# Optimization experiments

Measured on AMD Instinct MI355X. Metric: run time of the kernel, lower is better.

## Reference

```python
import jax, jax.numpy as jnp
import numpy as np

B, NPG, DEG = 128, 400, 16
N, E = B * NPG, B * NPG * DEG
E_PER = E // B
K1, K2, K3 = 360, 324, 292  # ceil(0.9*400), ceil(0.9*360), ceil(0.9*324)
EPS = 1e-5


def setup_inputs() -> dict:
    key = jax.random.key(0)
    ks = jax.random.split(key, 48)
    # edges constrained within each graph (contiguous equal-size graphs)
    g = jnp.repeat(jnp.arange(B, dtype=jnp.int32), E_PER)
    src = jax.random.randint(ks[0], (E,), 0, NPG, dtype=jnp.int32) + g * NPG
    dst = jax.random.randint(ks[1], (E,), 0, NPG, dtype=jnp.int32) + g * NPG
    inp = {
        'x': jax.random.normal(ks[2], (N, 64), dtype=jnp.float32),
        'edge_index': jnp.stack([src, dst]),
        'batch': jnp.repeat(jnp.arange(B, dtype=jnp.int32), NPG),
    }
    def glorot(k, a, b):
        lim = float(np.sqrt(6.0 / (a + b)))
        return jax.random.uniform(k, (a, b), minval=-lim, maxval=lim, dtype=jnp.float32)
    conv_dims = [(64, 32), (32, 64), (64, 128), (128, 128)]
    for i, (a, b) in enumerate(conv_dims, 1):
        inp[f'W{i}'] = glorot(ks[2 + i], a, b)
        inp[f'b{i}'] = jnp.zeros((b,), jnp.float32)
    for i, d in zip((1, 2, 3), (32, 64, 128)):
        inp[f'p{i}'] = jax.random.uniform(ks[8 + i], (d,), minval=-1.0, maxval=1.0, dtype=jnp.float32) / float(np.sqrt(d))
    lin_dims = [(128, 64), (64, 64), (64, 32), (32, 16), (16, 1)]
    for i, (a, b) in enumerate(lin_dims, 1):
        inp[f'Lw{i}'] = glorot(ks[12 + i], a, b)
        inp[f'Lb{i}'] = jnp.zeros((b,), jnp.float32)
    for i, d in enumerate((64, 64, 32, 16), 1):
        inp[f'g{i}'] = jnp.ones((d,), jnp.float32)
        inp[f'be{i}'] = jnp.zeros((d,), jnp.float32)
    return inp


def _gcn(x, src, dst, emask, nmask, W, b):
    h = x @ W
    deg = nmask + jax.ops.segment_sum(emask, dst, num_segments=N)
    dinv = jnp.where(deg > 0, jax.lax.rsqrt(deg), 0.0)
    norm = dinv[src] * dinv[dst] * emask
    agg = jax.ops.segment_sum(h[src] * norm[:, None], dst, num_segments=N)
    agg = agg + h * (dinv * dinv * nmask)[:, None]  # self-loop term
    return (agg + b) * nmask[:, None]


def _topk_pool(x, nmask, p, k):
    # PyG TopKPooling: score = x.p/||p||, keep top-k per graph, x *= tanh(score)
    score = (x @ p) / jnp.linalg.norm(p)
    sel = jnp.where(nmask > 0, score, -jnp.inf).reshape(B, NPG)
    _, idx = jax.lax.top_k(sel, k)
    gidx = (idx + (jnp.arange(B) * NPG)[:, None]).reshape(-1)
    new_mask = jnp.zeros((N,), x.dtype).at[gidx].set(1.0)
    return x * (jnp.tanh(score) * new_mask)[:, None], new_mask


def reference(x, edge_index, batch, W1, b1, p1, W2, b2, p2, W3, b3, p3, W4, b4,
              Lw1, Lb1, Lw2, Lb2, Lw3, Lb3, Lw4, Lb4, Lw5, Lb5,
              g1, be1, g2, be2, g3, be3, g4, be4):
    src, dst = edge_index[0], edge_index[1]
    nmask = jnp.ones((N,), jnp.float32)
    emask = jnp.ones((E,), jnp.float32)
    x = jax.nn.relu(_gcn(x, src, dst, emask, nmask, W1, b1))
    x, nmask = _topk_pool(x, nmask, p1, K1)
    emask = emask * nmask[src] * nmask[dst]
    x = jax.nn.relu(_gcn(x, src, dst, emask, nmask, W2, b2))
    x, nmask = _topk_pool(x, nmask, p2, K2)
    emask = emask * nmask[src] * nmask[dst]
    x = jax.nn.relu(_gcn(x, src, dst, emask, nmask, W3, b3))
    x, nmask = _topk_pool(x, nmask, p3, K3)
    emask = emask * nmask[src] * nmask[dst]
    x = jax.nn.relu(_gcn(x, src, dst, emask, nmask, W4, b4))
    h = x.reshape(B, NPG, -1).max(axis=1)
    def lin_bn(h, W, bb, ga, be):
        h = h @ W + bb
        m = h.mean(0)
        v = h.var(0)  # biased, matches BatchNorm1d training normalization
        return jax.nn.relu(ga * (h - m) / jnp.sqrt(v + EPS) + be)
    h = lin_bn(h, Lw1, Lb1, g1, be1)
    h = lin_bn(h, Lw2, Lb2, g2, be2)
    h = lin_bn(h, Lw3, Lb3, g3, be3)
    h = lin_bn(h, Lw4, Lb4, g4, be4)
    return h @ Lw5 + Lb5
```

## Files before the change

### kernel.cpp

```cpp
#include <hip/hip_runtime.h>
#include <math.h>

#define NNODES 51200
#define BGRAPHS 128
#define NPG 400
#define NEDGES 819200
#define EPG 6400
#define SLP 7680

__global__ __launch_bounds__(512) void csr_build_kernel(
    const int* __restrict__ src, const int* __restrict__ dst,
    unsigned short* __restrict__ slg, int* __restrict__ gsg, int* __restrict__ gcg,
    float* __restrict__ nmask, float* __restrict__ dinv, float* __restrict__ sc,
    float* __restrict__ hp) {
    __shared__ int deg[NPG];
    __shared__ int incl[512];
    __shared__ int gs[NPG];
    __shared__ int cur[NPG];
    const int g = blockIdx.x, t = threadIdx.x;
    for (int i = t; i < NPG; i += 512) deg[i] = 0;
    if (t < 128) hp[g * 128 + t] = 0.0f;
    __syncthreads();
    for (int e = t; e < EPG; e += 512)
        atomicAdd(&deg[dst[g * EPG + e] - g * NPG], 1);
    __syncthreads();
    const int d = (t < NPG) ? deg[t] : 0;
    const int p = (d + 3) >> 2;
    incl[t] = p;
    __syncthreads();
    for (int off = 1; off < 512; off <<= 1) {
        int add = (t >= off) ? incl[t - off] : 0;
        __syncthreads();
        incl[t] += add;
        __syncthreads();
    }
    if (t < NPG) {
        const int gstart = incl[t] - p;
        gs[t] = gstart;
        gsg[g * NPG + t] = gstart;
        gcg[g * NPG + t] = p;
        cur[t] = gstart * 4;
        nmask[g * NPG + t] = 1.0f;
        const float dv = rsqrtf(1.0f + (float)d);
        dinv[g * NPG + t] = dv;
        sc[g * NPG + t] = dv;
    }
    __syncthreads();
    for (int e = t; e < EPG; e += 512) {
        int dl = dst[g * EPG + e] - g * NPG;
        int pos = atomicAdd(&cur[dl], 1);
        slg[g * SLP + pos] = (unsigned short)(src[g * EPG + e] - g * NPG);
    }
    __syncthreads();
    if (t < NPG) {
        const int end = (gs[t] + p) * 4;
        for (int i = cur[t]; i < end; i++) slg[g * SLP + i] = (unsigned short)NPG;
    }
}

template<int IN, int OUT, int MODE>
__global__ __launch_bounds__(256) void gemm_kernel(
    const float* __restrict__ X, const float* __restrict__ W,
    const float* __restrict__ bias, const float* __restrict__ nmask,
    float* __restrict__ H, const float* __restrict__ p,
    float* __restrict__ score, float* __restrict__ hp) {
    __shared__ __align__(16) float sX[64 * IN];
    __shared__ unsigned smax[256];
    const int row0 = blockIdx.x * 64;
    const int t = threadIdx.x;
    for (int i = t; i < 64 * IN / 4; i += 256)
        reinterpret_cast<float4*>(sX)[i] =
            reinterpret_cast<const float4*>(X + (size_t)row0 * IN)[i];
    if (MODE == 3) smax[t] = 0u;
    __syncthreads();
    constexpr int CG  = OUT / 4;
    constexpr int RG  = 256 / CG;
    constexpr int RPT = 64 / RG;
    const int c0 = (t % CG) * 4;
    const int r0 = (t / CG) * RPT;
    float acc[RPT][4];
#pragma unroll
    for (int r = 0; r < RPT; r++)
#pragma unroll
        for (int j = 0; j < 4; j++) acc[r][j] = 0.0f;
    for (int k4 = 0; k4 < IN / 4; k4++) {
        const float4 w0 = *reinterpret_cast<const float4*>(&W[(k4 * 4 + 0) * OUT + c0]);
        const float4 w1 = *reinterpret_cast<const float4*>(&W[(k4 * 4 + 1) * OUT + c0]);
        const float4 w2 = *reinterpret_cast<const float4*>(&W[(k4 * 4 + 2) * OUT + c0]);
        const float4 w3 = *reinterpret_cast<const float4*>(&W[(k4 * 4 + 3) * OUT + c0]);
#pragma unroll
        for (int r = 0; r < RPT; r++) {
            const float4 xv = *reinterpret_cast<const float4*>(&sX[(r0 + r) * IN + k4 * 4]);
            acc[r][0] += xv.x * w0.x + xv.y * w1.x + xv.z * w2.x + xv.w * w3.x;
            acc[r][1] += xv.x * w0.y + xv.y * w1.y + xv.z * w2.y + xv.w * w3.y;
            acc[r][2] += xv.x * w0.z + xv.y * w1.z + xv.z * w2.z + xv.w * w3.z;
            acc[r][3] += xv.x * w0.w + xv.y * w1.w + xv.z * w2.w + xv.w * w3.w;
        }
    }
    const int graph0 = row0 / 400;
    const int bnd = (graph0 + 1) * 400;
    float ps[RPT];
    float cmax[4] = {0.f, 0.f, 0.f, 0.f};
#pragma unroll
    for (int r = 0; r < RPT; r++) {
        const int row = row0 + r0 + r;
        float4 v = make_float4(acc[r][0], acc[r][1], acc[r][2], acc[r][3]);
        if (MODE >= 2) {
            const float4 b4 = *reinterpret_cast<const float4*>(&bias[c0]);
            const float m = nmask[row];
            v.x = fmaxf(v.x + b4.x, 0.0f) * m;
            v.y = fmaxf(v.y + b4.y, 0.0f) * m;
            v.z = fmaxf(v.z + b4.z, 0.0f) * m;
            v.w = fmaxf(v.w + b4.w, 0.0f) * m;
        }
        if (MODE != 3) *reinterpret_cast<float4*>(&H[(size_t)row * OUT + c0]) = v;
        if (MODE == 2) {
            const float4 p4 = *reinterpret_cast<const float4*>(&p[c0]);
            ps[r] = v.x * p4.x + v.y * p4.y + v.z * p4.z + v.w * p4.w;
        }
        if (MODE == 3) {
            cmax[0] = fmaxf(cmax[0], v.x);
            cmax[1] = fmaxf(cmax[1], v.y);
            cmax[2] = fmaxf(cmax[2], v.z);
            cmax[3] = fmaxf(cmax[3], v.w);
        }
    }
    if (MODE == 2) {
#pragma unroll
        for (int r = 0; r < RPT; r++) {
#pragma unroll
            for (int off = 1; off < CG; off <<= 1) ps[r] += __shfl_xor(ps[r], off);
        }
        if ((t % CG) == 0) {
#pragma unroll
            for (int r = 0; r < RPT; r++) score[row0 + r0 + r] = ps[r];
        }
    }
    if (MODE == 3) {
        const int seg = ((row0 + r0) >= bnd) ? 1 : 0;
        atomicMax(&smax[seg * 128 + c0 + 0], __float_as_uint(cmax[0]));
        atomicMax(&smax[seg * 128 + c0 + 1], __float_as_uint(cmax[1]));
        atomicMax(&smax[seg * 128 + c0 + 2], __float_as_uint(cmax[2]));
        atomicMax(&smax[seg * 128 + c0 + 3], __float_as_uint(cmax[3]));
        __syncthreads();
        unsigned* hpu = reinterpret_cast<unsigned*>(hp);
        if (t < 128) atomicMax(&hpu[graph0 * 128 + t], smax[t]);
        const int graph1 = (row0 + 63) / 400;
        if (graph1 != graph0 && t < 128) atomicMax(&hpu[graph1 * 128 + t], smax[128 + t]);
    }
}

template<int OUT, int NCH, int NS, bool EPI, bool SCORE>
__global__ __launch_bounds__(512) void gcn_agg_kernel(
    const float* __restrict__ H, float* __restrict__ Y,
    const float* __restrict__ dinv, const float* __restrict__ sc,
    const float* __restrict__ bias, const float* __restrict__ p,
    float* __restrict__ score,
    const unsigned short* __restrict__ slg, const int* __restrict__ gsg,
    const int* __restrict__ gcg) {
    __shared__ __align__(16) float Hl[(NPG + 1) * 36];
    __shared__ float dinvl[NPG];
    __shared__ int gsl[NPG];
    __shared__ int gcl[NPG];
    __shared__ unsigned long long sl64[SLP / 4];
    const unsigned short* sl = reinterpret_cast<const unsigned short*>(sl64);
    const int b   = blockIdx.x;
    const int g   = b / (NCH * NS);
    const int rem = b % (NCH * NS);
    const int f0  = (rem / NS) * 32;
    const int n0  = (rem % NS) * (NPG / NS);
    const int t   = threadIdx.x;

    for (int i = t; i < NPG; i += 512) {
        dinvl[i] = dinv[g * NPG + i];
        gsl[i] = gsg[g * NPG + i];
        gcl[i] = gcg[g * NPG + i];
    }
    for (int i = t; i < SLP / 4; i += 512)
        sl64[i] = reinterpret_cast<const unsigned long long*>(slg + (size_t)g * SLP)[i];
    if (t < 36) Hl[NPG * 36 + t] = 0.0f;
    for (int i = t; i < NPG * 8; i += 512) {
        const int n = i >> 3, q = i & 7;
        const float s = sc[g * NPG + n];
        float4 v = *reinterpret_cast<const float4*>(&H[(size_t)(g * NPG + n) * OUT + f0 + q * 4]);
        v.x *= s; v.y *= s; v.z *= s; v.w *= s;
        *reinterpret_cast<float4*>(&Hl[n * 36 + q * 4]) = v;
    }
    __syncthreads();

    const int wave = t >> 6, lane = t & 63;
    const int sub = lane >> 3, f4 = lane & 7;
    constexpr int NPB = NPG / NS;
    for (int n = n0 + wave * 8 + sub; n < n0 + NPB; n += 64) {
        const float di = dinvl[n];
        if (di == 0.0f) continue;
        const int g0 = gsl[n], g1 = g0 + gcl[n];
        float4 acc = *reinterpret_cast<const float4*>(&Hl[n * 36 + f4 * 4]);
        for (int gg = g0; gg < g1; ++gg) {
            const unsigned long long q = *reinterpret_cast<const unsigned long long*>(&sl[gg * 4]);
            const int s0 = (int)(q & 0xFFFF), s1 = (int)((q >> 16) & 0xFFFF);
            const int s2 = (int)((q >> 32) & 0xFFFF), s3 = (int)(q >> 48);
            const float4 a = *reinterpret_cast<const float4*>(&Hl[s0 * 36 + f4 * 4]);
            const float4 bb = *reinterpret_cast<const float4*>(&Hl[s1 * 36 + f4 * 4]);
            const float4 c = *reinterpret_cast<const float4*>(&Hl[s2 * 36 + f4 * 4]);
            const float4 dd = *reinterpret_cast<const float4*>(&Hl[s3 * 36 + f4 * 4]);
            acc.x += (a.x + bb.x) + (c.x + dd.x);
            acc.y += (a.y + bb.y) + (c.y + dd.y);
            acc.z += (a.z + bb.z) + (c.z + dd.z);
            acc.w += (a.w + bb.w) + (c.w + dd.w);
        }
        acc.x *= di; acc.y *= di; acc.z *= di; acc.w *= di;
        if (EPI) {
            const float4 b4 = *reinterpret_cast<const float4*>(&bias[f0 + f4 * 4]);
            acc.x = fmaxf(acc.x + b4.x, 0.0f);
            acc.y = fmaxf(acc.y + b4.y, 0.0f);
            acc.z = fmaxf(acc.z + b4.z, 0.0f);
            acc.w = fmaxf(acc.w + b4.w, 0.0f);
        }
        *reinterpret_cast<float4*>(&Y[(size_t)(g * NPG + n) * OUT + f0 + f4 * 4]) = acc;
        if (SCORE) {
            const float4 p4 = *reinterpret_cast<const float4*>(&p[f4 * 4]);
            float part = acc.x * p4.x + acc.y * p4.y + acc.z * p4.z + acc.w * p4.w;
            part += __shfl_xor(part, 1);
            part += __shfl_xor(part, 2);
            part += __shfl_xor(part, 4);
            if (f4 == 0) score[g * NPG + n] = part;
        }
    }
}

template<int DIM>
__global__ __launch_bounds__(512) void topk_kernel(
    const float* __restrict__ score, float* __restrict__ nmask,
    float* __restrict__ dinv, float* __restrict__ sc,
    const float* __restrict__ p, int K,
    const unsigned short* __restrict__ slg, const int* __restrict__ gsg,
    const int* __restrict__ gcg) {
    __shared__ float sval[512];
    __shared__ int   sidx[512];
    __shared__ float sraw[NPG];
    __shared__ float nml[NPG + 1];
    __shared__ unsigned long long sl64[SLP / 4];
    __shared__ int gsl[NPG];
    __shared__ int gcl[NPG];
    __shared__ float spnorm;
    const unsigned short* sl = reinterpret_cast<const unsigned short*>(sl64);
    const int g = blockIdx.x;
    const int t = threadIdx.x;
    for (int i = t; i < SLP / 4; i += 512)
        sl64[i] = reinterpret_cast<const unsigned long long*>(slg + (size_t)g * SLP)[i];
    for (int i = t; i < NPG; i += 512) {
        gsl[i] = gsg[g * NPG + i];
        gcl[i] = gcg[g * NPG + i];
    }
    if (t == 0) {
        float s = 0.0f;
        for (int j = 0; j < DIM; j++) s += p[j] * p[j];
        spnorm = sqrtf(s);
    }
    float v = -INFINITY;
    int ix = t;
    if (t < NPG) {
        const float raw = score[g * NPG + t];
        sraw[t] = raw;
        v = (nmask[g * NPG + t] > 0.0f) ? raw : -INFINITY;
    }
    __syncthreads();
    for (int kk = 2; kk <= 512; kk <<= 1) {
        for (int j = kk >> 1; j > 0; j >>= 1) {
            float vb; int ib;
            if (j >= 64) {
                sval[t] = v; sidx[t] = ix;
                __syncthreads();
                vb = sval[t ^ j]; ib = sidx[t ^ j];
                __syncthreads();
            } else {
                vb = __shfl_xor(v, j, 64);
                ib = __shfl_xor(ix, j, 64);
            }
            const bool ownFirst = (v > vb) || (v == vb && ix < ib);
            const bool lower = (t & j) == 0;
            const bool desc = (t & kk) == 0;
            const bool keepOwn = lower ? (desc == ownFirst) : (desc != ownFirst);
            if (!keepOwn) { v = vb; ix = ib; }
        }
    }
    if (t <= NPG) nml[t] = 0.0f;
    __syncthreads();
    if (t < K) nml[ix] = 1.0f;
    __syncthreads();
    if (t < NPG) nmask[g * NPG + t] = nml[t];
    for (int n = t; n < NPG; n += 512) {
        float dv = 0.0f;
        if (nml[n] > 0.0f) {
            float d = 1.0f;
            const int g0 = gsl[n], g1 = g0 + gcl[n];
            for (int gg = g0; gg < g1; ++gg) {
                const unsigned long long q = *reinterpret_cast<const unsigned long long*>(&sl[gg * 4]);
                d += nml[(int)(q & 0xFFFF)] + nml[(int)((q >> 16) & 0xFFFF)] +
                     nml[(int)((q >> 32) & 0xFFFF)] + nml[(int)(q >> 48)];
            }
            dv = rsqrtf(d);
        }
        dinv[g * NPG + n] = dv;
        sc[g * NPG + n] = (nml[n] > 0.0f) ? tanhf(sraw[n] / spnorm) * dv : 0.0f;
    }
}

template<int IN, int OUT>
__global__ __launch_bounds__(128) void head_layer_kernel(
    const float* __restrict__ A, const float* __restrict__ W,
    const float* __restrict__ b, const float* __restrict__ ga,
    const float* __restrict__ be, float* __restrict__ Y) {
    __shared__ float Al[128 * (IN + 1)];
    __shared__ float red[4];
    const int c = blockIdx.x, t = threadIdx.x;
    for (int i = t; i < 128 * IN; i += 128)
        Al[(i / IN) * (IN + 1) + (i % IN)] = A[i];
    __syncthreads();
    float acc = b[c];
#pragma unroll
    for (int j = 0; j < IN; j++) acc += Al[t * (IN + 1) + j] * W[j * OUT + c];
    float s1 = acc, s2 = acc * acc;
    for (int o = 32; o > 0; o >>= 1) {
        s1 += __shfl_down(s1, o, 64);
        s2 += __shfl_down(s2, o, 64);
    }
    if ((t & 63) == 0) { red[t >> 6] = s1; red[2 + (t >> 6)] = s2; }
    __syncthreads();
    const float S1 = red[0] + red[1], S2 = red[2] + red[3];
    const float m = S1 * (1.0f / 128.0f);
    const float var = S2 * (1.0f / 128.0f) - m * m;
    float val = ga[c] * (acc - m) * rsqrtf(var + 1e-5f) + be[c];
    Y[t * OUT + c] = fmaxf(val, 0.0f);
}

__global__ __launch_bounds__(128) void head_final_kernel(
    const float* __restrict__ A, const float* __restrict__ w,
    const float* __restrict__ b, float* __restrict__ out) {
    const int t = threadIdx.x;
    float acc = b[0];
#pragma unroll
    for (int j = 0; j < 16; j++) acc += A[t * 16 + j] * w[j];
    out[t] = acc;
}

extern "C" void kernel_launch(void* const* d_in, const int* in_sizes, int n_in,
                              void* d_out, int out_size, void* d_ws, size_t ws_size,
                              hipStream_t stream) {
    (void)in_sizes; (void)n_in; (void)out_size; (void)ws_size;
    const float* x   = (const float*)d_in[0];
    const int*   ei  = (const int*)d_in[1];
    const float* W1  = (const float*)d_in[3];  const float* b1  = (const float*)d_in[4];
    const float* W2  = (const float*)d_in[5];  const float* b2  = (const float*)d_in[6];
    const float* W3  = (const float*)d_in[7];  const float* b3  = (const float*)d_in[8];
    const float* W4  = (const float*)d_in[9];  const float* b4  = (const float*)d_in[10];
    const float* p1  = (const float*)d_in[11];
    const float* p2  = (const float*)d_in[12];
    const float* p3  = (const float*)d_in[13];
    const float* Lw1 = (const float*)d_in[14]; const float* Lb1 = (const float*)d_in[15];
    const float* Lw2 = (const float*)d_in[16]; const float* Lb2 = (const float*)d_in[17];
    const float* Lw3 = (const float*)d_in[18]; const float* Lb3 = (const float*)d_in[19];
    const float* Lw4 = (const float*)d_in[20]; const float* Lb4 = (const float*)d_in[21];
    const float* Lw5 = (const float*)d_in[22]; const float* Lb5 = (const float*)d_in[23];
    const float* g1  = (const float*)d_in[24]; const float* be1 = (const float*)d_in[25];
    const float* g2  = (const float*)d_in[26]; const float* be2 = (const float*)d_in[27];
    const float* g3  = (const float*)d_in[28]; const float* be3 = (const float*)d_in[29];
    const float* g4  = (const float*)d_in[30]; const float* be4 = (const float*)d_in[31];

    const int* src = ei;
    const int* dst = ei + NEDGES;

    float* ws    = (float*)d_ws;
    float* hb    = ws;
    float* x0    = hb + (size_t)NNODES * 128;
    float* x1    = x0 + (size_t)NNODES * 128;
    float* nmask = x1 + (size_t)NNODES * 128;
    float* dinv  = nmask + NNODES;
    float* sc    = dinv + NNODES;
    float* scoreb= sc + NNODES;
    float* hp    = scoreb + NNODES;
    float* a1    = hp + 128 * 128;
    float* a2    = a1 + 128 * 64;
    float* a3    = a2 + 128 * 64;
    float* a4    = a3 + 128 * 32;
    unsigned short* slg = (unsigned short*)(a4 + 128 * 16);
    int* gsg = (int*)(slg + (size_t)BGRAPHS * SLP);
    int* gcg = gsg + (size_t)BGRAPHS * NPG;

    csr_build_kernel<<<BGRAPHS, 512, 0, stream>>>(src, dst, slg, gsg, gcg, nmask, dinv, sc, hp);

    gemm_kernel<64, 32, 0><<<NNODES / 64, 256, 0, stream>>>(x, W1, nullptr, nullptr, hb, nullptr, nullptr, nullptr);
    gcn_agg_kernel<32, 1, 2, true, true><<<BGRAPHS * 2, 512, 0, stream>>>(hb, x0, dinv, sc, b1, p1, scoreb, slg, gsg, gcg);
    topk_kernel<32><<<BGRAPHS, 512, 0, stream>>>(scoreb, nmask, dinv, sc, p1, 360, slg, gsg, gcg);

    gcn_agg_kernel<32, 1, 2, false, false><<<BGRAPHS * 2, 512, 0, stream>>>(x0, hb, dinv, sc, nullptr, nullptr, nullptr, slg, gsg, gcg);
    gemm_kernel<32, 64, 2><<<NNODES / 64, 256, 0, stream>>>(hb, W2, b2, nmask, x1, p2, scoreb, nullptr);
    topk_kernel<64><<<BGRAPHS, 512, 0, stream>>>(scoreb, nmask, dinv, sc, p2, 324, slg, gsg, gcg);

    gcn_agg_kernel<64, 2, 2, false, false><<<BGRAPHS * 4, 512, 0, stream>>>(x1, hb, dinv, sc, nullptr, nullptr, nullptr, slg, gsg, gcg);
    gemm_kernel<64, 128, 2><<<NNODES / 64, 256, 0, stream>>>(hb, W3, b3, nmask, x0, p3, scoreb, nullptr);
    topk_kernel<128><<<BGRAPHS, 512, 0, stream>>>(scoreb, nmask, dinv, sc, p3, 292, slg, gsg, gcg);

    gcn_agg_kernel<128, 4, 1, false, false><<<BGRAPHS * 4, 512, 0, stream>>>(x0, hb, dinv, sc, nullptr, nullptr, nullptr, slg, gsg, gcg);
    gemm_kernel<128, 128, 3><<<NNODES / 64, 256, 0, stream>>>(hb, W4, b4, nmask, x1, nullptr, nullptr, hp);

    head_layer_kernel<128, 64><<<64, 128, 0, stream>>>(hp, Lw1, Lb1, g1, be1, a1);
    head_layer_kernel<64, 64><<<64, 128, 0, stream>>>(a1, Lw2, Lb2, g2, be2, a2);
    head_layer_kernel<64, 32><<<32, 128, 0, stream>>>(a2, Lw3, Lb3, g3, be3, a3);
    head_layer_kernel<32, 16><<<16, 128, 0, stream>>>(a3, Lw4, Lb4, g4, be4, a4);
    head_final_kernel<<<1, 128, 0, stream>>>(a4, Lw5, Lb5, (float*)d_out);
}
```

Measured before the change: 204.9 us.

## Fuse top-k pooling into the following GCN aggregation kernel

Removes the standalone topk_kernel launches. Each aggregation block now recomputes the per-graph bitonic top-k, new node mask, degree normalisation and tanh score scale in shared memory before aggregating. The mask is double-buffered (nmA/nmB) so blocks can read the old mask while one block writes the new one. This removes three launches and the global round-trip for dinv and sc. In exchange, the sort is done redundantly by 2–4 blocks per graph, and each block's prologue gets longer.

```diff
diff --git a/kernel.cpp b/kernel.cpp
--- a/kernel.cpp
+++ b/kernel.cpp
@@ -150,19 +150,24 @@
     }
 }
 
-template<int OUT, int NCH, int NS, bool EPI, bool SCORE>
+template<int OUT, int NCH, int NS, bool EPI, bool SCORE, bool TOPK>
 __global__ __launch_bounds__(512) void gcn_agg_kernel(
     const float* __restrict__ H, float* __restrict__ Y,
-    const float* __restrict__ dinv, const float* __restrict__ sc,
-    const float* __restrict__ bias, const float* __restrict__ p,
-    float* __restrict__ score,
+    const float* __restrict__ dinv_g, const float* __restrict__ sc_g,
+    const float* __restrict__ bias,
+    const float* __restrict__ p_sc, float* __restrict__ score_out,
+    const float* __restrict__ scoreb_in, const float* __restrict__ nmask_in,
+    float* __restrict__ nmask_out, const float* __restrict__ p_pool,
+    int K, int PDIM,
     const unsigned short* __restrict__ slg, const int* __restrict__ gsg,
     const int* __restrict__ gcg) {
     __shared__ __align__(16) float Hl[(NPG + 1) * 36];
     __shared__ float dinvl[NPG];
+    __shared__ float scl[NPG];
     __shared__ int gsl[NPG];
     __shared__ int gcl[NPG];
     __shared__ unsigned long long sl64[SLP / 4];
+    __shared__ float misc[4];
     const unsigned short* sl = reinterpret_cast<const unsigned short*>(sl64);
     const int b   = blockIdx.x;
     const int g   = b / (NCH * NS);
@@ -172,20 +177,89 @@
     const int t   = threadIdx.x;
 
     for (int i = t; i < NPG; i += 512) {
-        dinvl[i] = dinv[g * NPG + i];
         gsl[i] = gsg[g * NPG + i];
         gcl[i] = gcg[g * NPG + i];
     }
     for (int i = t; i < SLP / 4; i += 512)
         sl64[i] = reinterpret_cast<const unsigned long long*>(slg + (size_t)g * SLP)[i];
-    if (t < 36) Hl[NPG * 36 + t] = 0.0f;
+
+    if (TOPK) {
+        float* sval = Hl;
+        int*   sidx = (int*)(Hl + 512);
+        float* sraw = Hl + 1024;
+        float* nml  = Hl + 1440;
+        if (t < 64) {
+            float s = 0.0f;
+            for (int j = t; j < PDIM; j += 64) s += p_pool[j] * p_pool[j];
+#pragma unroll
+            for (int o = 32; o > 0; o >>= 1) s += __shfl_xor(s, o, 64);
+            if (t == 0) misc[0] = sqrtf(s);
+        }
+        float v = -INFINITY;
+        int ix = t;
+        if (t < NPG) {
+            const float raw = scoreb_in[g * NPG + t];
+            sraw[t] = raw;
+            v = (nmask_in[g * NPG + t] > 0.0f) ? raw : -INFINITY;
+        }
+        __syncthreads();
+        for (int kk = 2; kk <= 512; kk <<= 1) {
+            for (int j = kk >> 1; j > 0; j >>= 1) {
+                float vb; int ib;
+                if (j >= 64) {
+                    sval[t] = v; sidx[t] = ix;
+                    __syncthreads();
+                    vb = sval[t ^ j]; ib = sidx[t ^ j];
+                    __syncthreads();
+                } else {
+                    vb = __shfl_xor(v, j, 64);
+                    ib = __shfl_xor(ix, j, 64);
+                }
+                const bool ownFirst = (v > vb) || (v == vb && ix < ib);
+                const bool lower = (t & j) == 0;
+                const bool desc = (t & kk) == 0;
+                const bool keepOwn = lower ? (desc == ownFirst) : (desc != ownFirst);
+                if (!keepOwn) { v = vb; ix = ib; }
+            }
+        }
+        if (t <= NPG) nml[t] = 0.0f;
+        __syncthreads();
+        if (t < K) nml[ix] = 1.0f;
+        __syncthreads();
+        if (rem == 0 && t < NPG) nmask_out[g * NPG + t] = nml[t];
+        const float spn = misc[0];
+        for (int n = t; n < NPG; n += 512) {
+            float dv = 0.0f;
+            if (nml[n] > 0.0f) {
+                float d = 1.0f;
+                const int g0 = gsl[n], g1 = g0 + gcl[n];
+                for (int gg = g0; gg < g1; ++gg) {
+                    const unsigned long long q = *reinterpret_cast<const unsigned long long*>(&sl[gg * 4]);
+                    d += nml[(int)(q & 0xFFFF)] + nml[(int)((q >> 16) & 0xFFFF)] +
+                         nml[(int)((q >> 32) & 0xFFFF)] + nml[(int)(q >> 48)];
+                }
+                dv = rsqrtf(d);
+            }
+            dinvl[n] = dv;
+            scl[n] = (nml[n] > 0.0f) ? tanhf(sraw[n] / spn) * dv : 0.0f;
+        }
+        __syncthreads();
+    } else {
+        for (int i = t; i < NPG; i += 512) {
+            dinvl[i] = dinv_g[g * NPG + i];
+            scl[i]   = sc_g[g * NPG + i];
+        }
+        __syncthreads();
+    }
+
     for (int i = t; i < NPG * 8; i += 512) {
         const int n = i >> 3, q = i & 7;
-        const float s = sc[g * NPG + n];
+        const float s = scl[n];
         float4 v = *reinterpret_cast<const float4*>(&H[(size_t)(g * NPG + n) * OUT + f0 + q * 4]);
         v.x *= s; v.y *= s; v.z *= s; v.w *= s;
         *reinterpret_cast<float4*>(&Hl[n * 36 + q * 4]) = v;
     }
+    if (t < 36) Hl[NPG * 36 + t] = 0.0f;
     __syncthreads();
 
     const int wave = t >> 6, lane = t & 63;
@@ -219,91 +293,13 @@
         }
         *reinterpret_cast<float4*>(&Y[(size_t)(g * NPG + n) * OUT + f0 + f4 * 4]) = acc;
         if (SCORE) {
-            const float4 p4 = *reinterpret_cast<const float4*>(&p[f4 * 4]);
+            const float4 p4 = *reinterpret_cast<const float4*>(&p_sc[f4 * 4]);
             float part = acc.x * p4.x + acc.y * p4.y + acc.z * p4.z + acc.w * p4.w;
             part += __shfl_xor(part, 1);
             part += __shfl_xor(part, 2);
             part += __shfl_xor(part, 4);
-            if (f4 == 0) score[g * NPG + n] = part;
-        }
-    }
-}
-
-template<int DIM>
-__global__ __launch_bounds__(512) void topk_kernel(
-    const float* __restrict__ score, float* __restrict__ nmask,
-    float* __restrict__ dinv, float* __restrict__ sc,
-    const float* __restrict__ p, int K,
-    const unsigned short* __restrict__ slg, const int* __restrict__ gsg,
-    const int* __restrict__ gcg) {
-    __shared__ float sval[512];
-    __shared__ int   sidx[512];
-    __shared__ float sraw[NPG];
-    __shared__ float nml[NPG + 1];
-    __shared__ unsigned long long sl64[SLP / 4];
-    __shared__ int gsl[NPG];
-    __shared__ int gcl[NPG];
-    __shared__ float spnorm;
-    const unsigned short* sl = reinterpret_cast<const unsigned short*>(sl64);
-    const int g = blockIdx.x;
-    const int t = threadIdx.x;
-    for (int i = t; i < SLP / 4; i += 512)
-        sl64[i] = reinterpret_cast<const unsigned long long*>(slg + (size_t)g * SLP)[i];
-    for (int i = t; i < NPG; i += 512) {
-        gsl[i] = gsg[g * NPG + i];
-        gcl[i] = gcg[g * NPG + i];
-    }
-    if (t == 0) {
-        float s = 0.0f;
-        for (int j = 0; j < DIM; j++) s += p[j] * p[j];
-        spnorm = sqrtf(s);
-    }
-    float v = -INFINITY;
-    int ix = t;
-    if (t < NPG) {
-        const float raw = score[g * NPG + t];
-        sraw[t] = raw;
-        v = (nmask[g * NPG + t] > 0.0f) ? raw : -INFINITY;
-    }
-    __syncthreads();
-    for (int kk = 2; kk <= 512; kk <<= 1) {
-        for (int j = kk >> 1; j > 0; j >>= 1) {
-            float vb; int ib;
-            if (j >= 64) {
-                sval[t] = v; sidx[t] = ix;
-                __syncthreads();
-                vb = sval[t ^ j]; ib = sidx[t ^ j];
-                __syncthreads();
-            } else {
-                vb = __shfl_xor(v, j, 64);
-                ib = __shfl_xor(ix, j, 64);
-            }
-            const bool ownFirst = (v > vb) || (v == vb && ix < ib);
-            const bool lower = (t & j) == 0;
-            const bool desc = (t & kk) == 0;
-            const bool keepOwn = lower ? (desc == ownFirst) : (desc != ownFirst);
-            if (!keepOwn) { v = vb; ix = ib; }
-        }
-    }
-    if (t <= NPG) nml[t] = 0.0f;
-    __syncthreads();
-    if (t < K) nml[ix] = 1.0f;
-    __syncthreads();
-    if (t < NPG) nmask[g * NPG + t] = nml[t];
-    for (int n = t; n < NPG; n += 512) {
-        float dv = 0.0f;
-        if (nml[n] > 0.0f) {
-            float d = 1.0f;
-            const int g0 = gsl[n], g1 = g0 + gcl[n];
-            for (int gg = g0; gg < g1; ++gg) {
-                const unsigned long long q = *reinterpret_cast<const unsigned long long*>(&sl[gg * 4]);
-                d += nml[(int)(q & 0xFFFF)] + nml[(int)((q >> 16) & 0xFFFF)] +
-                     nml[(int)((q >> 32) & 0xFFFF)] + nml[(int)(q >> 48)];
-            }
-            dv = rsqrtf(d);
-        }
-        dinv[g * NPG + n] = dv;
-        sc[g * NPG + n] = (nml[n] > 0.0f) ? tanhf(sraw[n] / spnorm) * dv : 0.0f;
+            if (f4 == 0) score_out[g * NPG + n] = part;
+        }
     }
 }
 
@@ -375,8 +371,9 @@
     float* hb    = ws;
     float* x0    = hb + (size_t)NNODES * 128;
     float* x1    = x0 + (size_t)NNODES * 128;
-    float* nmask = x1 + (size_t)NNODES * 128;
-    float* dinv  = nmask + NNODES;
+    float* nmA   = x1 + (size_t)NNODES * 128;
+    float* nmB   = nmA + NNODES;
+    float* dinv  = nmB + NNODES;
     float* sc    = dinv + NNODES;
     float* scoreb= sc + NNODES;
     float* hp    = scoreb + NNODES;
@@ -388,22 +385,27 @@
     int* gsg = (int*)(slg + (size_t)BGRAPHS * SLP);
     int* gcg = gsg + (size_t)BGRAPHS * NPG;
 
-    csr_build_kernel<<<BGRAPHS, 512, 0, stream>>>(src, dst, slg, gsg, gcg, nmask, dinv, sc, hp);
+    csr_build_kernel<<<BGRAPHS, 512, 0, stream>>>(src, dst, slg, gsg, gcg, nmA, dinv, sc, hp);
 
     gemm_kernel<64, 32, 0><<<NNODES / 64, 256, 0, stream>>>(x, W1, nullptr, nullptr, hb, nullptr, nullptr, nullptr);
-    gcn_agg_kernel<32, 1, 2, true, true><<<BGRAPHS * 2, 512, 0, stream>>>(hb, x0, dinv, sc, b1, p1, scoreb, slg, gsg, gcg);
-    topk_kernel<32><<<BGRAPHS, 512, 0, stream>>>(scoreb, nmask, dinv, sc, p1, 360, slg, gsg, gcg);
-
-    gcn_agg_kernel<32, 1, 2, false, false><<<BGRAPHS * 2, 512, 0, stream>>>(x0, hb, dinv, sc, nullptr, nullptr, nullptr, slg, gsg, gcg);
-    gemm_kernel<32, 64, 2><<<NNODES / 64, 256, 0, stream>>>(hb, W2, b2, nmask, x1, p2, scoreb, nullptr);
-    topk_kernel<64><<<BGRAPHS, 512, 0, stream>>>(scoreb, nmask, dinv, sc, p2, 324, slg, gsg, gcg);
-
-    gcn_agg_kernel<64, 2, 2, false, false><<<BGRAPHS * 4, 512, 0, stream>>>(x1, hb, dinv, sc, nullptr, nullptr, nullptr, slg, gsg, gcg);
-    gemm_kernel<64, 128, 2><<<NNODES / 64, 256, 0, stream>>>(hb, W3, b3, nmask, x0, p3, scoreb, nullptr);
-    topk_kernel<128><<<BGRAPHS, 512, 0, stream>>>(scoreb, nmask, dinv, sc, p3, 292, slg, gsg, gcg);
-
-    gcn_agg_kernel<128, 4, 1, false, false><<<BGRAPHS * 4, 512, 0, stream>>>(x0, hb, dinv, sc, nullptr, nullptr, nullptr, slg, gsg, gcg);
-    gemm_kernel<128, 128, 3><<<NNODES / 64, 256, 0, stream>>>(hb, W4, b4, nmask, x1, nullptr, nullptr, hp);
+    gcn_agg_kernel<32, 1, 2, true, true, false><<<BGRAPHS * 2, 512, 0, stream>>>(
+        hb, x0, dinv, sc, b1, p1, scoreb,
+        nullptr, nullptr, nullptr, nullptr, 0, 0, slg, gsg, gcg);
+
+    gcn_agg_kernel<32, 1, 2, false, false, true><<<BGRAPHS * 2, 512, 0, stream>>>(
+        x0, hb, nullptr, nullptr, nullptr, nullptr, nullptr,
+        scoreb, nmA, nmB, p1, 360, 32, slg, gsg, gcg);
+    gemm_kernel<32, 64, 2><<<NNODES / 64, 256, 0, stream>>>(hb, W2, b2, nmB, x1, p2, scoreb, nullptr);
+
+    gcn_agg_kernel<64, 2, 2, false, false, true><<<BGRAPHS * 4, 512, 0, stream>>>(
+        x1, hb, nullptr, nullptr, nullptr, nullptr, nullptr,
+        scoreb, nmB, nmA, p2, 324, 64, slg, gsg, gcg);
+    gemm_kernel<64, 128, 2><<<NNODES / 64, 256, 0, stream>>>(hb, W3, b3, nmA, x0, p3, scoreb, nullptr);
+
+    gcn_agg_kernel<128, 4, 1, false, false, true><<<BGRAPHS * 4, 512, 0, stream>>>(
+        x0, hb, nullptr, nullptr, nullptr, nullptr, nullptr,
+        scoreb, nmA, nmB, p3, 292, 128, slg, gsg, gcg);
+    gemm_kernel<128, 128, 3><<<NNODES / 64, 256, 0, stream>>>(hb, W4, b4, nmB, x1, nullptr, nullptr, hp);
 
     head_layer_kernel<128, 64><<<64, 128, 0, stream>>>(hp, Lw1, Lb1, g1, be1, a1);
     head_layer_kernel<64, 64><<<64, 128, 0, stream>>>(a1, Lw2, Lb2, g2, be2, a2);
```

Result: faster. 197.1 us (-3.8%).
